# Kernel optimization log

Hardware: AMD Instinct MI355X
Metric: run time of the kernel (lower is better)

Reference implementation:

```python
import jax, jax.numpy as jnp
import numpy as np

N, E, G = 100000, 800000, 1
DV, DE, DU, H = 64, 32, 32, 128

def _w(key, shape):
    return jax.random.normal(key, shape, dtype=jnp.float32) * 0.05

def setup_inputs() -> dict:
    key = jax.random.key(0)
    ks = jax.random.split(key, 16)
    inp = {
        "node_attr": jax.random.normal(ks[0], (N, DV), dtype=jnp.float32),
        "edges": jax.random.randint(ks[1], (2, E), 0, N, dtype=jnp.int64 if jax.config.jax_enable_x64 else jnp.int32),
        "edge_attr": jax.random.normal(ks[2], (E, DE), dtype=jnp.float32),
        "u": jax.random.normal(ks[3], (G, DU), dtype=jnp.float32),
        "node_idx": jnp.zeros((N,), dtype=jnp.int32),
        "edge_idx": jnp.zeros((E,), dtype=jnp.int32),
        # edge MLP: concat(src, dst, edge_attr, u) -> H -> H
        "W1e": _w(ks[4], (2 * DV + DE + DU, H)), "b1e": jnp.zeros((H,), jnp.float32),
        "W2e": _w(ks[5], (H, H)), "b2e": jnp.zeros((H,), jnp.float32),
        # node MLP: concat(node_attr, aggregated_edges, u) -> H -> H
        "W1n": _w(ks[6], (DV + H + DU, H)), "b1n": jnp.zeros((H,), jnp.float32),
        "W2n": _w(ks[7], (H, H)), "b2n": jnp.zeros((H,), jnp.float32),
        # global MLP: concat(node_mean, edge_mean, u) -> H -> H
        "W1g": _w(ks[8], (H + H + DU, H)), "b1g": jnp.zeros((H,), jnp.float32),
        "W2g": _w(ks[9], (H, H)), "b2g": jnp.zeros((H,), jnp.float32),
    }
    return inp

def _mlp(x, W1, b1, W2, b2):
    return jax.nn.relu(x @ W1 + b1) @ W2 + b2

def _seg_mean(x, seg, num):
    s = jax.ops.segment_sum(x, seg, num_segments=num)
    c = jax.ops.segment_sum(jnp.ones((x.shape[0], 1), x.dtype), seg, num_segments=num)
    return s / jnp.maximum(c, 1.0)

def reference(node_attr, edges, edge_attr, u, node_idx, edge_idx,
              W1e, b1e, W2e, b2e, W1n, b1n, W2n, b2n, W1g, b1g, W2g, b2g):
    row, col = edges[0], edges[1]
    # edge model: gather endpoint features, concat with edge/global attrs
    e_in = jnp.concatenate([node_attr[row], node_attr[col], edge_attr, u[edge_idx]], axis=-1)
    e = _mlp(e_in, W1e, b1e, W2e, b2e)                        # [E, H]
    # node model: scatter-add incoming edge messages onto receivers (col)
    agg = jax.ops.segment_sum(e, col, num_segments=node_attr.shape[0])  # [N, H]
    v_in = jnp.concatenate([node_attr, agg, u[node_idx]], axis=-1)
    v = _mlp(v_in, W1n, b1n, W2n, b2n)                        # [N, H]
    # global model: per-graph mean pooling of nodes and edges
    nv = _seg_mean(v, node_idx, u.shape[0])                   # [G, H]
    ne = _seg_mean(e, edge_idx, u.shape[0])                   # [G, H]
    g_in = jnp.concatenate([nv, ne, u], axis=-1)
    g = _mlp(g_in, W1g, b1g, W2g, b2g)                        # [G, H]
    return v, e, g
```

## Files before the change

kernel.cpp:

```cpp
#include <hip/hip_runtime.h>

#define N_NODES 100000
#define N_EDGES 800000
#define DV 64
#define DE 32
#define DU 32
#define H 128

#define NTILES 12500

typedef short bf16x8 __attribute__((ext_vector_type(8)));
typedef unsigned short u16;
typedef u16 u16x8 __attribute__((ext_vector_type(8)));
typedef float f32x4 __attribute__((ext_vector_type(4)));

#define OFF_ESUM  0
#define OFF_VSUM  8192
#define OFF_PART  16384
#define OFF_WBUF  18432
#define OFF_DEG   190464
#define OFF_OFFS  590464
#define OFF_BUCK  990464
#define OFF_DSTP  4190464
#define OFF_SRCP  7390464
#define OFF_EIDXP 10590464

#define W1ET_OFF 0
#define W2ET_OFF 24576
#define W1NT_OFF 40960
#define W2NT_OFF 69632
#define WBUF_ELEMS 86016

#define NPART 391

__device__ inline u16 f2bf(float x) {
  union { float f; unsigned u; } c; c.f = x;
  unsigned r = c.u + 0x7FFFu + ((c.u >> 16) & 1u);
  return (u16)(r >> 16);
}

__global__ void prep_weights(const float* __restrict__ W1e, const float* __restrict__ W2e,
                             const float* __restrict__ W1n, const float* __restrict__ W2n,
                             u16* __restrict__ wbuf) {
  int i = blockIdx.x * blockDim.x + threadIdx.x;
  if (i < 24576) {
    int j = i / 192, k = i - j * 192;
    wbuf[W1ET_OFF + i] = f2bf(W1e[k * H + j]);
  } else if (i < 40960) {
    int t = i - 24576; int j = t >> 7, k = t & 127;
    wbuf[i] = f2bf(W2e[k * H + j]);
  } else if (i < 69632) {
    int t = i - 40960; int j = t / 224, k = t - j * 224;
    wbuf[i] = f2bf(W1n[k * H + j]);
  } else if (i < WBUF_ELEMS) {
    int t = i - 69632; int j = t >> 7, k = t & 127;
    wbuf[i] = f2bf(W2n[k * H + j]);
  }
}

__global__ void degree_kernel(const int* __restrict__ edges, int* __restrict__ deg) {
  int i = blockIdx.x * 256 + threadIdx.x;
  if (i < N_EDGES) atomicAdd(&deg[edges[N_EDGES + i]], 1);
}

__global__ void scan_part(const int* __restrict__ deg, int* __restrict__ part) {
  int i = blockIdx.x * 256 + threadIdx.x;
  int v = (i < N_NODES) ? deg[i] : 0;
#pragma unroll
  for (int m = 1; m < 64; m <<= 1) v += __shfl_xor(v, m);
  __shared__ int s[4];
  if ((threadIdx.x & 63) == 0) s[threadIdx.x >> 6] = v;
  __syncthreads();
  if (threadIdx.x == 0) part[blockIdx.x] = s[0] + s[1] + s[2] + s[3];
}

__global__ void scan_top(int* __restrict__ part) {
  __shared__ int s[512];
  int t = threadIdx.x;
  s[t] = (t < NPART) ? part[t] : 0;
  __syncthreads();
  for (int d = 1; d < 512; d <<= 1) {
    int v = (t >= d) ? s[t - d] : 0;
    __syncthreads();
    s[t] += v;
    __syncthreads();
  }
  if (t < NPART) part[t] = (t == 0) ? 0 : s[t - 1];
}

__global__ void scan_down(const int* __restrict__ part, int* __restrict__ deg_cursor,
                          int* __restrict__ offsets) {
  __shared__ int s[256];
  int b = blockIdx.x, t = threadIdx.x;
  int i = b * 256 + t;
  int v = (i < N_NODES) ? deg_cursor[i] : 0;
  s[t] = v;
  __syncthreads();
  for (int d = 1; d < 256; d <<= 1) {
    int u = (t >= d) ? s[t - d] : 0;
    __syncthreads();
    s[t] += u;
    __syncthreads();
  }
  int excl = s[t] - v + part[b];
  if (i < N_NODES) { offsets[i] = excl; deg_cursor[i] = excl; }
}

__global__ void fill_kernel(const int* __restrict__ edges, const int* __restrict__ edge_idx,
                            int* __restrict__ cursor, int* __restrict__ bucket,
                            int* __restrict__ dstP, int* __restrict__ srcP,
                            int* __restrict__ eidxP) {
  int i = blockIdx.x * 256 + threadIdx.x;
  if (i < N_EDGES) {
    int s = edges[i];
    int d = edges[N_EDGES + i];
    int pos = atomicAdd(&cursor[d], 1);
    bucket[pos] = i;
    dstP[pos] = d;
    srcP[pos] = s;
    eidxP[pos] = edge_idx[i];
  }
}

__global__ __launch_bounds__(256, 3) void edge_kernel(
    const float* __restrict__ node_attr, const float* __restrict__ edge_attr,
    const float* __restrict__ uattr, const u16* __restrict__ wbuf,
    const float* __restrict__ b1, const float* __restrict__ b2,
    const int* __restrict__ bucket, const int* __restrict__ dstP,
    const int* __restrict__ srcP, const int* __restrict__ eidxP,
    float* __restrict__ e_out, float* __restrict__ agg, float* __restrict__ esum_p)
{
  __shared__ __align__(16) char smem[43008];
  u16 (*X)[200]    = (u16(*)[200])smem;
  u16 (*Hs)[136]   = (u16(*)[136])(smem + 25600);
  float (*OT)[132] = (float(*)[132])smem;
  __shared__ int sSrc[64], sDst[64], sEid[64], sEidx[64];

  const int tid = threadIdx.x;
  const int wave = tid >> 6, lane = tid & 63;
  const int l15 = lane & 15, lg = lane >> 4;
  const int wc = wave * 32;

  int b = blockIdx.x;
  const int q = NTILES / 8, r8 = NTILES % 8;
  int xcd = b & 7, pos = b >> 3;
  long t = (xcd < r8 ? xcd * (q + 1) : r8 * (q + 1) + (xcd - r8) * q) + pos;
  const long i0 = t * 64;

  if (tid < 64)        sSrc[tid]        = srcP[i0 + tid];
  else if (tid < 128)  sDst[tid - 64]   = dstP[i0 + (tid - 64)];
  else if (tid < 192)  sEid[tid - 128]  = bucket[i0 + (tid - 128)];
  else                 sEidx[tid - 192] = eidxP[i0 + (tid - 192)];

  bf16x8 w1[6][2], w2[4][2];
  {
    const u16* w1t = wbuf + W1ET_OFF;
    const u16* w2t = wbuf + W2ET_OFF;
#pragma unroll
    for (int cf = 0; cf < 2; ++cf) {
      const u16* p1 = w1t + (wc + cf * 16 + l15) * 192 + lg * 8;
#pragma unroll
      for (int ks = 0; ks < 6; ++ks) w1[ks][cf] = *(const bf16x8*)(p1 + ks * 32);
      const u16* p2 = w2t + (wc + cf * 16 + l15) * 128 + lg * 8;
#pragma unroll
      for (int ks = 0; ks < 4; ++ks) w2[ks][cf] = *(const bf16x8*)(p2 + ks * 32);
    }
  }

  __syncthreads();

#pragma unroll
  for (int it = 0; it < 6; ++it) {
    int ch = tid + it * 256;
    int r = ch / 24, seg = ch - r * 24;
    int col = seg * 8;
    const float* src;
    if (col < 64)        src = node_attr + (long)sSrc[r] * DV + col;
    else if (col < 128)  src = node_attr + (long)sDst[r] * DV + (col - 64);
    else if (col < 160)  src = edge_attr + (long)sEid[r] * DE + (col - 128);
    else                 src = uattr + (long)sEidx[r] * DU + (col - 160);
    float4 f0 = *(const float4*)src;
    float4 f1 = *(const float4*)(src + 4);
    u16x8 p;
    p[0] = f2bf(f0.x); p[1] = f2bf(f0.y); p[2] = f2bf(f0.z); p[3] = f2bf(f0.w);
    p[4] = f2bf(f1.x); p[5] = f2bf(f1.y); p[6] = f2bf(f1.z); p[7] = f2bf(f1.w);
    *(u16x8*)&X[r][col] = p;
  }

  __syncthreads();

  f32x4 acc[4][2];
#pragma unroll
  for (int rf = 0; rf < 4; ++rf)
#pragma unroll
    for (int cf = 0; cf < 2; ++cf)
#pragma unroll
      for (int j = 0; j < 4; ++j) acc[rf][cf][j] = 0.f;

#pragma unroll
  for (int ks = 0; ks < 6; ++ks) {
#pragma unroll
    for (int rf = 0; rf < 4; ++rf) {
      bf16x8 a = *(const bf16x8*)&X[rf * 16 + l15][ks * 32 + lg * 8];
      acc[rf][0] = __builtin_amdgcn_mfma_f32_16x16x32_bf16(a, w1[ks][0], acc[rf][0], 0, 0, 0);
      acc[rf][1] = __builtin_amdgcn_mfma_f32_16x16x32_bf16(a, w1[ks][1], acc[rf][1], 0, 0, 0);
    }
  }

  float bias1[2] = { b1[wc + l15], b1[wc + 16 + l15] };
#pragma unroll
  for (int rf = 0; rf < 4; ++rf)
#pragma unroll
    for (int cf = 0; cf < 2; ++cf)
#pragma unroll
      for (int j = 0; j < 4; ++j) {
        float hv = acc[rf][cf][j] + bias1[cf];
        hv = hv > 0.f ? hv : 0.f;
        Hs[rf * 16 + lg * 4 + j][wc + cf * 16 + l15] = f2bf(hv);
      }

  __syncthreads();

#pragma unroll
  for (int rf = 0; rf < 4; ++rf)
#pragma unroll
    for (int cf = 0; cf < 2; ++cf)
#pragma unroll
      for (int j = 0; j < 4; ++j) acc[rf][cf][j] = 0.f;

#pragma unroll
  for (int ks = 0; ks < 4; ++ks) {
#pragma unroll
    for (int rf = 0; rf < 4; ++rf) {
      bf16x8 a = *(const bf16x8*)&Hs[rf * 16 + l15][ks * 32 + lg * 8];
      acc[rf][0] = __builtin_amdgcn_mfma_f32_16x16x32_bf16(a, w2[ks][0], acc[rf][0], 0, 0, 0);
      acc[rf][1] = __builtin_amdgcn_mfma_f32_16x16x32_bf16(a, w2[ks][1], acc[rf][1], 0, 0, 0);
    }
  }

  __syncthreads();

  float bias2[2] = { b2[wc + l15], b2[wc + 16 + l15] };
  float es0 = 0.f, es1 = 0.f;
#pragma unroll
  for (int rf = 0; rf < 4; ++rf) {
#pragma unroll
    for (int cf = 0; cf < 2; ++cf) {
#pragma unroll
      for (int j = 0; j < 4; ++j) {
        float v = acc[rf][cf][j] + bias2[cf];
        OT[rf * 16 + lg * 4 + j][wc + cf * 16 + l15] = v;
        if (cf == 0) es0 += v; else es1 += v;
      }
    }
  }

  __syncthreads();

  if (tid < 128) {
    const int c = tid;
    float sum = OT[0][c];
    int runStart = 0;
    int dprev = sDst[0];
    for (int r = 1; r < 64; ++r) {
      int d = sDst[r];
      if (d != dprev) {
        if (runStart == 0) atomicAdd(&agg[(long)dprev * H + c], sum);
        else               agg[(long)dprev * H + c] = sum;
        runStart = r; sum = 0.f; dprev = d;
      }
      sum += OT[r][c];
    }
    atomicAdd(&agg[(long)dprev * H + c], sum);
  } else {
#pragma unroll
    for (int i = 0; i < 16; ++i) {
      int ch = (tid - 128) + i * 128;
      int r = ch >> 5, c4 = ch & 31;
      float4 f = *(const float4*)&OT[r][c4 * 4];
      *(float4*)(e_out + (long)sEid[r] * H + c4 * 4) = f;
    }
  }

#pragma unroll
  for (int m = 16; m < 64; m <<= 1) { es0 += __shfl_xor(es0, m); es1 += __shfl_xor(es1, m); }
  if (lane < 16) {
    atomicAdd(&esum_p[(wc + lane) * 16], es0);
    atomicAdd(&esum_p[(wc + 16 + lane) * 16], es1);
  }
}

__global__ __launch_bounds__(256, 3) void node_kernel(
    const float* __restrict__ node_attr, const float* __restrict__ uattr,
    const int* __restrict__ node_idx, const u16* __restrict__ wbuf,
    const float* __restrict__ b1, const float* __restrict__ b2,
    float* __restrict__ vio, float* __restrict__ vsum_p)
{
  __shared__ __align__(16) u16 X[64][232];
  __shared__ __align__(16) u16 Hs[64][136];

  const int tid = threadIdx.x;
  const int wave = tid >> 6, lane = tid & 63;
  const int l15 = lane & 15, lg = lane >> 4;
  const long n0 = (long)blockIdx.x * 64;
  const int wc = wave * 32;

#pragma unroll
  for (int it = 0; it < 7; ++it) {
    int ch = tid + it * 256;
    int r = ch / 28, seg = ch - r * 28;
    int col = seg * 8;
    long n = n0 + r; if (n >= N_NODES) n = N_NODES - 1;
    const float* src;
    if (col < 64)        src = node_attr + n * DV + col;
    else if (col < 192)  src = vio + n * H + (col - 64);
    else                 src = uattr + (long)node_idx[n] * DU + (col - 192);
    float4 f0 = *(const float4*)src;
    float4 f1 = *(const float4*)(src + 4);
    u16x8 p;
    p[0] = f2bf(f0.x); p[1] = f2bf(f0.y); p[2] = f2bf(f0.z); p[3] = f2bf(f0.w);
    p[4] = f2bf(f1.x); p[5] = f2bf(f1.y); p[6] = f2bf(f1.z); p[7] = f2bf(f1.w);
    *(u16x8*)&X[r][col] = p;
  }

  bf16x8 w1[7][2], w2[4][2];
  {
    const u16* w1t = wbuf + W1NT_OFF;
    const u16* w2t = wbuf + W2NT_OFF;
#pragma unroll
    for (int cf = 0; cf < 2; ++cf) {
      const u16* p1 = w1t + (wc + cf * 16 + l15) * 224 + lg * 8;
#pragma unroll
      for (int ks = 0; ks < 7; ++ks) w1[ks][cf] = *(const bf16x8*)(p1 + ks * 32);
      const u16* p2 = w2t + (wc + cf * 16 + l15) * 128 + lg * 8;
#pragma unroll
      for (int ks = 0; ks < 4; ++ks) w2[ks][cf] = *(const bf16x8*)(p2 + ks * 32);
    }
  }

  __syncthreads();

  f32x4 acc[4][2];
#pragma unroll
  for (int rf = 0; rf < 4; ++rf)
#pragma unroll
    for (int cf = 0; cf < 2; ++cf)
#pragma unroll
      for (int j = 0; j < 4; ++j) acc[rf][cf][j] = 0.f;

#pragma unroll
  for (int ks = 0; ks < 7; ++ks) {
#pragma unroll
    for (int rf = 0; rf < 4; ++rf) {
      bf16x8 a = *(const bf16x8*)&X[rf * 16 + l15][ks * 32 + lg * 8];
      acc[rf][0] = __builtin_amdgcn_mfma_f32_16x16x32_bf16(a, w1[ks][0], acc[rf][0], 0, 0, 0);
      acc[rf][1] = __builtin_amdgcn_mfma_f32_16x16x32_bf16(a, w1[ks][1], acc[rf][1], 0, 0, 0);
    }
  }

  float bias1[2] = { b1[wc + l15], b1[wc + 16 + l15] };
#pragma unroll
  for (int rf = 0; rf < 4; ++rf)
#pragma unroll
    for (int cf = 0; cf < 2; ++cf)
#pragma unroll
      for (int j = 0; j < 4; ++j) {
        float hv = acc[rf][cf][j] + bias1[cf];
        hv = hv > 0.f ? hv : 0.f;
        Hs[rf * 16 + lg * 4 + j][wc + cf * 16 + l15] = f2bf(hv);
      }

  __syncthreads();

#pragma unroll
  for (int rf = 0; rf < 4; ++rf)
#pragma unroll
    for (int cf = 0; cf < 2; ++cf)
#pragma unroll
      for (int j = 0; j < 4; ++j) acc[rf][cf][j] = 0.f;

#pragma unroll
  for (int ks = 0; ks < 4; ++ks) {
#pragma unroll
    for (int rf = 0; rf < 4; ++rf) {
      bf16x8 a = *(const bf16x8*)&Hs[rf * 16 + l15][ks * 32 + lg * 8];
      acc[rf][0] = __builtin_amdgcn_mfma_f32_16x16x32_bf16(a, w2[ks][0], acc[rf][0], 0, 0, 0);
      acc[rf][1] = __builtin_amdgcn_mfma_f32_16x16x32_bf16(a, w2[ks][1], acc[rf][1], 0, 0, 0);
    }
  }

  float bias2[2] = { b2[wc + l15], b2[wc + 16 + l15] };
  float vs0 = 0.f, vs1 = 0.f;
#pragma unroll
  for (int rf = 0; rf < 4; ++rf) {
#pragma unroll
    for (int cf = 0; cf < 2; ++cf) {
      int colg = wc + cf * 16 + l15;
#pragma unroll
      for (int j = 0; j < 4; ++j) {
        int r = rf * 16 + lg * 4 + j;
        long n = n0 + r;
        if (n < N_NODES) {
          float v = acc[rf][cf][j] + bias2[cf];
          vio[n * H + colg] = v;
          if (cf == 0) vs0 += v; else vs1 += v;
        }
      }
    }
  }
#pragma unroll
  for (int m = 16; m < 64; m <<= 1) { vs0 += __shfl_xor(vs0, m); vs1 += __shfl_xor(vs1, m); }
  if (lane < 16) {
    atomicAdd(&vsum_p[(wc + lane) * 16], vs0);
    atomicAdd(&vsum_p[(wc + 16 + lane) * 16], vs1);
  }
}

__global__ void global_kernel(const float* __restrict__ uattr,
    const float* __restrict__ W1g, const float* __restrict__ b1g,
    const float* __restrict__ W2g, const float* __restrict__ b2g,
    const float* __restrict__ esum_p, const float* __restrict__ vsum_p,
    float* __restrict__ g_out)
{
  __shared__ float gin[288];
  __shared__ float hbuf[128];
  int t = threadIdx.x;
  gin[t]       = vsum_p[t * 16] * (1.f / (float)N_NODES);
  gin[128 + t] = esum_p[t * 16] * (1.f / (float)N_EDGES);
  if (t < 32) gin[256 + t] = uattr[t];
  __syncthreads();
  float a = b1g[t];
  for (int k = 0; k < 288; ++k) a += gin[k] * W1g[k * H + t];
  hbuf[t] = fmaxf(a, 0.f);
  __syncthreads();
  float b = b2g[t];
  for (int k = 0; k < 128; ++k) b += hbuf[k] * W2g[k * H + t];
  g_out[t] = b;
}

extern "C" void kernel_launch(void* const* d_in, const int* in_sizes, int n_in,
                              void* d_out, int out_size, void* d_ws, size_t ws_size,
                              hipStream_t stream) {
  const float* node_attr = (const float*)d_in[0];
  const int*   edges     = (const int*)d_in[1];
  const float* edge_attr = (const float*)d_in[2];
  const float* uattr     = (const float*)d_in[3];
  const int*   node_idx  = (const int*)d_in[4];
  const int*   edge_idx  = (const int*)d_in[5];
  const float* W1e = (const float*)d_in[6];  const float* b1e = (const float*)d_in[7];
  const float* W2e = (const float*)d_in[8];  const float* b2e = (const float*)d_in[9];
  const float* W1n = (const float*)d_in[10]; const float* b1n = (const float*)d_in[11];
  const float* W2n = (const float*)d_in[12]; const float* b2n = (const float*)d_in[13];
  const float* W1g = (const float*)d_in[14]; const float* b1g = (const float*)d_in[15];
  const float* W2g = (const float*)d_in[16]; const float* b2g = (const float*)d_in[17];

  float* out   = (float*)d_out;
  float* v_out = out;
  float* e_out = out + (long)N_NODES * H;
  float* g_out = out + (long)N_NODES * H + (long)N_EDGES * H;

  char* ws = (char*)d_ws;
  float* esum_p = (float*)(ws + OFF_ESUM);
  float* vsum_p = (float*)(ws + OFF_VSUM);
  int*   part   = (int*)(ws + OFF_PART);
  u16*   wbuf   = (u16*)(ws + OFF_WBUF);
  int*   deg    = (int*)(ws + OFF_DEG);
  int*   offs   = (int*)(ws + OFF_OFFS);
  int*   buck   = (int*)(ws + OFF_BUCK);
  int*   dstP   = (int*)(ws + OFF_DSTP);
  int*   srcP   = (int*)(ws + OFF_SRCP);
  int*   eidxP  = (int*)(ws + OFF_EIDXP);

  hipMemsetAsync(ws, 0, 16384, stream);
  hipMemsetAsync(deg, 0, N_NODES * sizeof(int), stream);
  hipMemsetAsync(v_out, 0, (size_t)N_NODES * H * sizeof(float), stream);

  prep_weights<<<WBUF_ELEMS / 256, 256, 0, stream>>>(W1e, W2e, W1n, W2n, wbuf);
  degree_kernel<<<(N_EDGES + 255) / 256, 256, 0, stream>>>(edges, deg);
  scan_part<<<NPART, 256, 0, stream>>>(deg, part);
  scan_top<<<1, 512, 0, stream>>>(part);
  scan_down<<<NPART, 256, 0, stream>>>(part, deg, offs);
  fill_kernel<<<(N_EDGES + 255) / 256, 256, 0, stream>>>(edges, edge_idx, deg,
                                                         buck, dstP, srcP, eidxP);

  edge_kernel<<<NTILES, 256, 0, stream>>>(node_attr, edge_attr, uattr, wbuf,
                                          b1e, b2e, buck, dstP, srcP, eidxP,
                                          e_out, v_out, esum_p);
  node_kernel<<<(N_NODES + 63) / 64, 256, 0, stream>>>(node_attr, uattr, node_idx,
                                                       wbuf, b1n, b2n, v_out, vsum_p);
  global_kernel<<<1, 128, 0, stream>>>(uattr, W1g, b1g, W2g, b2g, esum_p, vsum_p, g_out);
}
```

Baseline: 630.1 us.

## Fold global attribute into first-layer biases and slim edge index buffers

Because there is a single graph, the u-contribution to the first layer of the edge and node MLPs is precomputed into per-layer bias vectors by a tiny kernel. This drops the u columns from the MFMA K dimension (192→160 for edges, 224→192 for nodes) and removes the u and edge_idx/node_idx gathers. The CSR fill now packs (src, edge id) into one int2 array and drops the eidx and offset arrays. In the edge kernel, occupancy is raised to 4 blocks, the W2 load is deferred until after GEMM1, and the segmented scatter-add is split across all 256 threads. This relies on G=1, so every graph index is 0, and adds a few more atomics at the half-tile boundaries.

```diff
diff --git a/kernel.cpp b/kernel.cpp
--- a/kernel.cpp
+++ b/kernel.cpp
@@ -14,22 +14,20 @@
 typedef u16 u16x8 __attribute__((ext_vector_type(8)));
 typedef float f32x4 __attribute__((ext_vector_type(4)));
 
-#define OFF_ESUM  0
-#define OFF_VSUM  8192
-#define OFF_PART  16384
-#define OFF_WBUF  18432
-#define OFF_DEG   190464
-#define OFF_OFFS  590464
-#define OFF_BUCK  990464
-#define OFF_DSTP  4190464
-#define OFF_SRCP  7390464
-#define OFF_EIDXP 10590464
+#define OFF_ESUM 0
+#define OFF_VSUM 8192
+#define OFF_BIAS 16384
+#define OFF_PART 17408
+#define OFF_WBUF 19456
+#define OFF_DEG  175104
+#define OFF_SE   575104
+#define OFF_DSTP 6975104
 
 #define W1ET_OFF 0
-#define W2ET_OFF 24576
-#define W1NT_OFF 40960
-#define W2NT_OFF 69632
-#define WBUF_ELEMS 86016
+#define W2ET_OFF 20480
+#define W1NT_OFF 36864
+#define W2NT_OFF 61440
+#define WBUF_ELEMS 77824
 
 #define NPART 391
 
@@ -43,19 +41,35 @@
                              const float* __restrict__ W1n, const float* __restrict__ W2n,
                              u16* __restrict__ wbuf) {
   int i = blockIdx.x * blockDim.x + threadIdx.x;
-  if (i < 24576) {
-    int j = i / 192, k = i - j * 192;
+  if (i < 20480) {
+    int j = i / 160, k = i - j * 160;
     wbuf[W1ET_OFF + i] = f2bf(W1e[k * H + j]);
-  } else if (i < 40960) {
-    int t = i - 24576; int j = t >> 7, k = t & 127;
+  } else if (i < 36864) {
+    int t = i - 20480; int j = t >> 7, k = t & 127;
     wbuf[i] = f2bf(W2e[k * H + j]);
-  } else if (i < 69632) {
-    int t = i - 40960; int j = t / 224, k = t - j * 224;
+  } else if (i < 61440) {
+    int t = i - 36864; int j = t / 192, k = t - j * 192;
     wbuf[i] = f2bf(W1n[k * H + j]);
   } else if (i < WBUF_ELEMS) {
-    int t = i - 69632; int j = t >> 7, k = t & 127;
+    int t = i - 61440; int j = t >> 7, k = t & 127;
     wbuf[i] = f2bf(W2n[k * H + j]);
   }
+}
+
+__global__ void prep_bias(const float* __restrict__ uattr,
+                          const float* __restrict__ W1e, const float* __restrict__ b1e,
+                          const float* __restrict__ W1n, const float* __restrict__ b1n,
+                          float* __restrict__ bias) {
+  int t = threadIdx.x;
+  float be = b1e[t];
+  float bn = b1n[t];
+  for (int k = 0; k < DU; ++k) {
+    float uk = uattr[k];
+    be += uk * W1e[(2 * DV + DE + k) * H + t];
+    bn += uk * W1n[(DV + H + k) * H + t];
+  }
+  bias[t] = be;
+  bias[128 + t] = bn;
 }
 
 __global__ void degree_kernel(const int* __restrict__ edges, int* __restrict__ deg) {
@@ -88,8 +102,7 @@
   if (t < NPART) part[t] = (t == 0) ? 0 : s[t - 1];
 }
 
-__global__ void scan_down(const int* __restrict__ part, int* __restrict__ deg_cursor,
-                          int* __restrict__ offsets) {
+__global__ void scan_down(const int* __restrict__ part, int* __restrict__ deg_cursor) {
   __shared__ int s[256];
   int b = blockIdx.x, t = threadIdx.x;
   int i = b * 256 + t;
@@ -103,38 +116,33 @@
     __syncthreads();
   }
   int excl = s[t] - v + part[b];
-  if (i < N_NODES) { offsets[i] = excl; deg_cursor[i] = excl; }
-}
-
-__global__ void fill_kernel(const int* __restrict__ edges, const int* __restrict__ edge_idx,
-                            int* __restrict__ cursor, int* __restrict__ bucket,
-                            int* __restrict__ dstP, int* __restrict__ srcP,
-                            int* __restrict__ eidxP) {
+  if (i < N_NODES) deg_cursor[i] = excl;
+}
+
+__global__ void fill_kernel(const int* __restrict__ edges, int* __restrict__ cursor,
+                            int2* __restrict__ se, int* __restrict__ dstP) {
   int i = blockIdx.x * 256 + threadIdx.x;
   if (i < N_EDGES) {
     int s = edges[i];
     int d = edges[N_EDGES + i];
     int pos = atomicAdd(&cursor[d], 1);
-    bucket[pos] = i;
+    se[pos] = make_int2(s, i);
     dstP[pos] = d;
-    srcP[pos] = s;
-    eidxP[pos] = edge_idx[i];
-  }
-}
-
-__global__ __launch_bounds__(256, 3) void edge_kernel(
+  }
+}
+
+__global__ __launch_bounds__(256, 4) void edge_kernel(
     const float* __restrict__ node_attr, const float* __restrict__ edge_attr,
-    const float* __restrict__ uattr, const u16* __restrict__ wbuf,
-    const float* __restrict__ b1, const float* __restrict__ b2,
-    const int* __restrict__ bucket, const int* __restrict__ dstP,
-    const int* __restrict__ srcP, const int* __restrict__ eidxP,
+    const u16* __restrict__ wbuf, const float* __restrict__ bias_f,
+    const float* __restrict__ b2,
+    const int2* __restrict__ se, const int* __restrict__ dstP,
     float* __restrict__ e_out, float* __restrict__ agg, float* __restrict__ esum_p)
 {
-  __shared__ __align__(16) char smem[43008];
-  u16 (*X)[200]    = (u16(*)[200])smem;
-  u16 (*Hs)[136]   = (u16(*)[136])(smem + 25600);
+  __shared__ __align__(16) char smem[37888];
+  u16 (*X)[164]    = (u16(*)[164])smem;
+  u16 (*Hs)[132]   = (u16(*)[132])(smem + 20992);
   float (*OT)[132] = (float(*)[132])smem;
-  __shared__ int sSrc[64], sDst[64], sEid[64], sEidx[64];
+  __shared__ int sSrc[64], sEid[64], sDst[64];
 
   const int tid = threadIdx.x;
   const int wave = tid >> 6, lane = tid & 63;
@@ -147,38 +155,32 @@
   long t = (xcd < r8 ? xcd * (q + 1) : r8 * (q + 1) + (xcd - r8) * q) + pos;
   const long i0 = t * 64;
 
-  if (tid < 64)        sSrc[tid]        = srcP[i0 + tid];
-  else if (tid < 128)  sDst[tid - 64]   = dstP[i0 + (tid - 64)];
-  else if (tid < 192)  sEid[tid - 128]  = bucket[i0 + (tid - 128)];
-  else                 sEidx[tid - 192] = eidxP[i0 + (tid - 192)];
-
-  bf16x8 w1[6][2], w2[4][2];
+  if (tid < 64)        { int2 v = se[i0 + tid]; sSrc[tid] = v.x; sEid[tid] = v.y; }
+  else if (tid < 128)  sDst[tid - 64] = dstP[i0 + (tid - 64)];
+
+  bf16x8 w1[5][2];
   {
     const u16* w1t = wbuf + W1ET_OFF;
-    const u16* w2t = wbuf + W2ET_OFF;
 #pragma unroll
     for (int cf = 0; cf < 2; ++cf) {
-      const u16* p1 = w1t + (wc + cf * 16 + l15) * 192 + lg * 8;
-#pragma unroll
-      for (int ks = 0; ks < 6; ++ks) w1[ks][cf] = *(const bf16x8*)(p1 + ks * 32);
-      const u16* p2 = w2t + (wc + cf * 16 + l15) * 128 + lg * 8;
-#pragma unroll
-      for (int ks = 0; ks < 4; ++ks) w2[ks][cf] = *(const bf16x8*)(p2 + ks * 32);
-    }
-  }
-
-  __syncthreads();
-
-#pragma unroll
-  for (int it = 0; it < 6; ++it) {
+      const u16* p1 = w1t + (wc + cf * 16 + l15) * 160 + lg * 8;
+#pragma unroll
+      for (int ks = 0; ks < 5; ++ks) w1[ks][cf] = *(const bf16x8*)(p1 + ks * 32);
+    }
+  }
+  float bias1[2] = { bias_f[wc + l15], bias_f[wc + 16 + l15] };
+
+  __syncthreads();
+
+#pragma unroll
+  for (int it = 0; it < 5; ++it) {
     int ch = tid + it * 256;
-    int r = ch / 24, seg = ch - r * 24;
-    int col = seg * 8;
+    int r = ch / 20, g = ch - r * 20;
+    int col = g * 8;
     const float* src;
     if (col < 64)        src = node_attr + (long)sSrc[r] * DV + col;
     else if (col < 128)  src = node_attr + (long)sDst[r] * DV + (col - 64);
-    else if (col < 160)  src = edge_attr + (long)sEid[r] * DE + (col - 128);
-    else                 src = uattr + (long)sEidx[r] * DU + (col - 160);
+    else                 src = edge_attr + (long)sEid[r] * DE + (col - 128);
     float4 f0 = *(const float4*)src;
     float4 f1 = *(const float4*)(src + 4);
     u16x8 p;
@@ -198,7 +200,7 @@
       for (int j = 0; j < 4; ++j) acc[rf][cf][j] = 0.f;
 
 #pragma unroll
-  for (int ks = 0; ks < 6; ++ks) {
+  for (int ks = 0; ks < 5; ++ks) {
 #pragma unroll
     for (int rf = 0; rf < 4; ++rf) {
       bf16x8 a = *(const bf16x8*)&X[rf * 16 + l15][ks * 32 + lg * 8];
@@ -207,7 +209,18 @@
     }
   }
 
-  float bias1[2] = { b1[wc + l15], b1[wc + 16 + l15] };
+  bf16x8 w2[4][2];
+  {
+    const u16* w2t = wbuf + W2ET_OFF;
+#pragma unroll
+    for (int cf = 0; cf < 2; ++cf) {
+      const u16* p2 = w2t + (wc + cf * 16 + l15) * 128 + lg * 8;
+#pragma unroll
+      for (int ks = 0; ks < 4; ++ks) w2[ks][cf] = *(const bf16x8*)(p2 + ks * 32);
+    }
+  }
+  float bias2[2] = { b2[wc + l15], b2[wc + 16 + l15] };
+
 #pragma unroll
   for (int rf = 0; rf < 4; ++rf)
 #pragma unroll
@@ -240,7 +253,6 @@
 
   __syncthreads();
 
-  float bias2[2] = { b2[wc + l15], b2[wc + 16 + l15] };
   float es0 = 0.f, es1 = 0.f;
 #pragma unroll
   for (int rf = 0; rf < 4; ++rf) {
@@ -257,28 +269,29 @@
 
   __syncthreads();
 
-  if (tid < 128) {
-    const int c = tid;
-    float sum = OT[0][c];
-    int runStart = 0;
-    int dprev = sDst[0];
-    for (int r = 1; r < 64; ++r) {
-      int d = sDst[r];
-      if (d != dprev) {
-        if (runStart == 0) atomicAdd(&agg[(long)dprev * H + c], sum);
-        else               agg[(long)dprev * H + c] = sum;
-        runStart = r; sum = 0.f; dprev = d;
+#pragma unroll
+  for (int i = 0; i < 8; ++i) {
+    int ch = tid + i * 256;
+    int r = ch >> 5, c4 = ch & 31;
+    float4 f = *(const float4*)&OT[r][c4 * 4];
+    *(float4*)(e_out + (long)sEid[r] * H + c4 * 4) = f;
+  }
+
+  {
+    const int c = tid & 127;
+    const int rlo = (tid >> 7) * 32;
+    float sum = 0.f;
+    int runStart = rlo;
+#pragma unroll 8
+    for (int r = rlo; r < rlo + 32; ++r) {
+      sum += OT[r][c];
+      bool bnd = (r == rlo + 31) || (sDst[r + 1] != sDst[r]);
+      if (bnd) {
+        float* p = &agg[(long)sDst[r] * H + c];
+        if (runStart == rlo || r == rlo + 31) atomicAdd(p, sum);
+        else *p = sum;
+        sum = 0.f; runStart = r + 1;
       }
-      sum += OT[r][c];
-    }
-    atomicAdd(&agg[(long)dprev * H + c], sum);
-  } else {
-#pragma unroll
-    for (int i = 0; i < 16; ++i) {
-      int ch = (tid - 128) + i * 128;
-      int r = ch >> 5, c4 = ch & 31;
-      float4 f = *(const float4*)&OT[r][c4 * 4];
-      *(float4*)(e_out + (long)sEid[r] * H + c4 * 4) = f;
     }
   }
 
@@ -291,13 +304,12 @@
 }
 
 __global__ __launch_bounds__(256, 3) void node_kernel(
-    const float* __restrict__ node_attr, const float* __restrict__ uattr,
-    const int* __restrict__ node_idx, const u16* __restrict__ wbuf,
-    const float* __restrict__ b1, const float* __restrict__ b2,
+    const float* __restrict__ node_attr, const u16* __restrict__ wbuf,
+    const float* __restrict__ bias_f, const float* __restrict__ b2,
     float* __restrict__ vio, float* __restrict__ vsum_p)
 {
-  __shared__ __align__(16) u16 X[64][232];
-  __shared__ __align__(16) u16 Hs[64][136];
+  __shared__ __align__(16) u16 X[64][196];
+  __shared__ __align__(16) u16 Hs[64][132];
 
   const int tid = threadIdx.x;
   const int wave = tid >> 6, lane = tid & 63;
@@ -306,15 +318,14 @@
   const int wc = wave * 32;
 
 #pragma unroll
-  for (int it = 0; it < 7; ++it) {
+  for (int it = 0; it < 6; ++it) {
     int ch = tid + it * 256;
-    int r = ch / 28, seg = ch - r * 28;
-    int col = seg * 8;
+    int r = ch / 24, g = ch - r * 24;
+    int col = g * 8;
     long n = n0 + r; if (n >= N_NODES) n = N_NODES - 1;
     const float* src;
-    if (col < 64)        src = node_attr + n * DV + col;
-    else if (col < 192)  src = vio + n * H + (col - 64);
-    else                 src = uattr + (long)node_idx[n] * DU + (col - 192);
+    if (col < 64)  src = node_attr + n * DV + col;
+    else           src = vio + n * H + (col - 64);
     float4 f0 = *(const float4*)src;
     float4 f1 = *(const float4*)(src + 4);
     u16x8 p;
@@ -323,15 +334,15 @@
     *(u16x8*)&X[r][col] = p;
   }
 
-  bf16x8 w1[7][2], w2[4][2];
+  bf16x8 w1[6][2], w2[4][2];
   {
     const u16* w1t = wbuf + W1NT_OFF;
     const u16* w2t = wbuf + W2NT_OFF;
 #pragma unroll
     for (int cf = 0; cf < 2; ++cf) {
-      const u16* p1 = w1t + (wc + cf * 16 + l15) * 224 + lg * 8;
-#pragma unroll
-      for (int ks = 0; ks < 7; ++ks) w1[ks][cf] = *(const bf16x8*)(p1 + ks * 32);
+      const u16* p1 = w1t + (wc + cf * 16 + l15) * 192 + lg * 8;
+#pragma unroll
+      for (int ks = 0; ks < 6; ++ks) w1[ks][cf] = *(const bf16x8*)(p1 + ks * 32);
       const u16* p2 = w2t + (wc + cf * 16 + l15) * 128 + lg * 8;
 #pragma unroll
       for (int ks = 0; ks < 4; ++ks) w2[ks][cf] = *(const bf16x8*)(p2 + ks * 32);
@@ -349,7 +360,7 @@
       for (int j = 0; j < 4; ++j) acc[rf][cf][j] = 0.f;
 
 #pragma unroll
-  for (int ks = 0; ks < 7; ++ks) {
+  for (int ks = 0; ks < 6; ++ks) {
 #pragma unroll
     for (int rf = 0; rf < 4; ++rf) {
       bf16x8 a = *(const bf16x8*)&X[rf * 16 + l15][ks * 32 + lg * 8];
@@ -358,7 +369,7 @@
     }
   }
 
-  float bias1[2] = { b1[wc + l15], b1[wc + 16 + l15] };
+  float bias1[2] = { bias_f[128 + wc + l15], bias_f[128 + wc + 16 + l15] };
 #pragma unroll
   for (int rf = 0; rf < 4; ++rf)
 #pragma unroll
@@ -445,8 +456,6 @@
   const int*   edges     = (const int*)d_in[1];
   const float* edge_attr = (const float*)d_in[2];
   const float* uattr     = (const float*)d_in[3];
-  const int*   node_idx  = (const int*)d_in[4];
-  const int*   edge_idx  = (const int*)d_in[5];
   const float* W1e = (const float*)d_in[6];  const float* b1e = (const float*)d_in[7];
   const float* W2e = (const float*)d_in[8];  const float* b2e = (const float*)d_in[9];
   const float* W1n = (const float*)d_in[10]; const float* b1n = (const float*)d_in[11];
@@ -462,31 +471,29 @@
   char* ws = (char*)d_ws;
   float* esum_p = (float*)(ws + OFF_ESUM);
   float* vsum_p = (float*)(ws + OFF_VSUM);
+  float* bias_f = (float*)(ws + OFF_BIAS);
   int*   part   = (int*)(ws + OFF_PART);
   u16*   wbuf   = (u16*)(ws + OFF_WBUF);
   int*   deg    = (int*)(ws + OFF_DEG);
-  int*   offs   = (int*)(ws + OFF_OFFS);
-  int*   buck   = (int*)(ws + OFF_BUCK);
+  int2*  se     = (int2*)(ws + OFF_SE);
   int*   dstP   = (int*)(ws + OFF_DSTP);
-  int*   srcP   = (int*)(ws + OFF_SRCP);
-  int*   eidxP  = (int*)(ws + OFF_EIDXP);
 
   hipMemsetAsync(ws, 0, 16384, stream);
   hipMemsetAsync(deg, 0, N_NODES * sizeof(int), stream);
   hipMemsetAsync(v_out, 0, (size_t)N_NODES * H * sizeof(float), stream);
 
   prep_weights<<<WBUF_ELEMS / 256, 256, 0, stream>>>(W1e, W2e, W1n, W2n, wbuf);
+  prep_bias<<<1, 128, 0, stream>>>(uattr, W1e, b1e, W1n, b1n, bias_f);
   degree_kernel<<<(N_EDGES + 255) / 256, 256, 0, stream>>>(edges, deg);
   scan_part<<<NPART, 256, 0, stream>>>(deg, part);
   scan_top<<<1, 512, 0, stream>>>(part);
-  scan_down<<<NPART, 256, 0, stream>>>(part, deg, offs);
-  fill_kernel<<<(N_EDGES + 255) / 256, 256, 0, stream>>>(edges, edge_idx, deg,
-                                                         buck, dstP, srcP, eidxP);
-
-  edge_kernel<<<NTILES, 256, 0, stream>>>(node_attr, edge_attr, uattr, wbuf,
-                                          b1e, b2e, buck, dstP, srcP, eidxP,
+  scan_down<<<NPART, 256, 0, stream>>>(part, deg);
+  fill_kernel<<<(N_EDGES + 255) / 256, 256, 0, stream>>>(edges, deg, se, dstP);
+
+  edge_kernel<<<NTILES, 256, 0, stream>>>(node_attr, edge_attr, wbuf,
+                                          bias_f, b2e, se, dstP,
                                           e_out, v_out, esum_p);
-  node_kernel<<<(N_NODES + 63) / 64, 256, 0, stream>>>(node_attr, uattr, node_idx,
-                                                       wbuf, b1n, b2n, v_out, vsum_p);
+  node_kernel<<<(N_NODES + 63) / 64, 256, 0, stream>>>(node_attr, wbuf,
+                                                       bias_f, b2n, v_out, vsum_p);
   global_kernel<<<1, 128, 0, stream>>>(uattr, W1g, b1g, W2g, b2g, esum_p, vsum_p, g_out);
 }
```

New measurement: 665.3 us. 5.6% more time.
